# Optimization experiments

Measured on AMD Instinct MI355X. Metric: run time of the kernel, lower is better.

The kernel has to match this reference:

```python
import jax, jax.numpy as jnp
from jax import lax
import numpy as np

FEAT = 2048
HID = 512
OUT = 22
B, T = 16, 2048


def _kaiming(key, shape):
    fan_in = shape[1]
    std = np.sqrt(2.0 / fan_in)
    return jax.random.normal(key, shape, dtype=jnp.float32) * std


def setup_inputs() -> dict:
    key = jax.random.key(0)
    ks = jax.random.split(key, 12)
    x = jax.random.normal(ks[0], (B, T, FEAT), dtype=jnp.float32)
    inp = {
        "x": x,
        # main cell (PyTorch LSTMCell gate order: i, f, g, o)
        "w_ih": _kaiming(ks[1], (4 * HID, FEAT)),
        "w_hh": _kaiming(ks[2], (4 * HID, HID)),
        "b_ih": jax.random.uniform(ks[3], (4 * HID,), minval=-0.04, maxval=0.04),
        "b_hh": jax.random.uniform(ks[4], (4 * HID,), minval=-0.04, maxval=0.04),
        # ed cell
        "w_ih_ed": _kaiming(ks[5], (4 * HID, FEAT)),
        "w_hh_ed": _kaiming(ks[6], (4 * HID, HID)),
        "b_ih_ed": jax.random.uniform(ks[7], (4 * HID,), minval=-0.04, maxval=0.04),
        "b_hh_ed": jax.random.uniform(ks[8], (4 * HID,), minval=-0.04, maxval=0.04),
        # linear heads
        "fc_w": _kaiming(ks[9], (OUT, HID)),
        "fc_b": jnp.zeros((OUT,), dtype=jnp.float32),
        "fc_ed_w": _kaiming(ks[10], (OUT, HID)),
        "fc_ed_b": jnp.zeros((OUT,), dtype=jnp.float32),
    }
    return inp


def _run_lstm(x, w_ih, w_hh, b_ih, b_hh):
    # Precompute input projection for all timesteps: [B, T, 4H]
    xg = jnp.einsum("btf,gf->btg", x, w_ih) + (b_ih + b_hh)
    hid = w_hh.shape[1]
    b = x.shape[0]

    def step(carry, xg_t):
        h, c = carry
        g = xg_t + h @ w_hh.T  # [B, 4H]
        i, f, gg, o = jnp.split(g, 4, axis=-1)
        c = jax.nn.sigmoid(f) * c + jax.nn.sigmoid(i) * jnp.tanh(gg)
        h = jax.nn.sigmoid(o) * jnp.tanh(c)
        return (h, c), h

    init = (jnp.zeros((b, hid), x.dtype), jnp.zeros((b, hid), x.dtype))
    _, hs = lax.scan(step, init, jnp.swapaxes(xg, 0, 1))  # hs: [T, B, H]
    return jnp.swapaxes(hs, 0, 1)  # [B, T, H]


def reference(x, w_ih, w_hh, b_ih, b_hh, w_ih_ed, w_hh_ed, b_ih_ed, b_hh_ed,
              fc_w, fc_b, fc_ed_w, fc_ed_b):
    hs = _run_lstm(x, w_ih, w_hh, b_ih, b_hh)
    score = jnp.einsum("bth,oh->bto", hs, fc_w) + fc_b
    hs_ed = _run_lstm(x, w_ih_ed, w_hh_ed, b_ih_ed, b_hh_ed)
    ed = jnp.einsum("bth,oh->bto", hs_ed, fc_ed_w) + fc_ed_b
    return (score, ed)
```

## Files before the change

### kernel.cpp

```cpp
#include <hip/hip_runtime.h>
#include <hip/hip_bf16.h>
#include <stdint.h>

typedef __attribute__((ext_vector_type(8))) short s16x8;
typedef __attribute__((ext_vector_type(4))) float f32x4;
typedef unsigned short u16;
typedef unsigned int u32;
typedef unsigned long long u64;

#define FEAT 2048
#define HID  512
#define GATES 2048
#define NB   16
#define NT   2048
#define NOUT 22
#define MROWS (NB*NT)

#define WS_FLAG 0L
#define WS_BIAS 4096L
#define WS_WF   (WS_BIAS + 16384L)
#define WS_WB   (WS_WF + 4194304L)
#define WS_XB   (WS_WB + 16777216L)
#define WS_XG   (WS_XB + 134217728L)
#define WS_HB   (WS_XG + 268435456L)
#define HB_BYTES 67141632L
#define HB_LSTM_U64 (2049L*2048L)
#define HB_SLAB_U64 2048L

__device__ inline float b2f(u16 u){ u32 x = ((u32)u) << 16; return __builtin_bit_cast(float, x); }
__device__ inline u16 f2b(float f){
  u32 u = __builtin_bit_cast(u32, f);
  u32 r = (u + 0x7FFFu + ((u >> 16) & 1u)) >> 16;
  return (u16)r;
}
__device__ inline float sigm(float x){ return __builtin_amdgcn_rcpf(1.f + __expf(-x)); }
__device__ inline float tanh_(float x){ return 1.f - 2.f*__builtin_amdgcn_rcpf(1.f + __expf(2.f*x)); }

__global__ void detect_dtype(const u32* __restrict__ x, int* __restrict__ flag){
  __shared__ int cs;
  if (threadIdx.x == 0) cs = 0;
  __syncthreads();
  int c = 0;
  for (int i = 0; i < 16; i++){
    u32 w = x[threadIdx.x*16 + i];
    u32 e = (w >> 7) & 0xFFu;
    if ((e >= 110u && e <= 134u) || ((w & 0xFFFFu) == 0u)) c++;
  }
  atomicAdd(&cs, c);
  __syncthreads();
  if (threadIdx.x == 0) *flag = (cs > 2048) ? 1 : 0;
}

__global__ void cvt_bf16(const void* __restrict__ src, u16* __restrict__ dst,
                         long n8, const int* __restrict__ flag){
  const int isb = *flag;
  long stride = (long)gridDim.x * blockDim.x;
  for (long i = (long)blockIdx.x*blockDim.x + threadIdx.x; i < n8; i += stride){
    if (isb){
      ((int4*)dst)[i] = ((const int4*)src)[i];
    } else {
      const float4* s = (const float4*)src + 2*i;
      float4 a = s[0], b = s[1];
      s16x8 o;
      o[0]=(short)f2b(a.x); o[1]=(short)f2b(a.y); o[2]=(short)f2b(a.z); o[3]=(short)f2b(a.w);
      o[4]=(short)f2b(b.x); o[5]=(short)f2b(b.y); o[6]=(short)f2b(b.z); o[7]=(short)f2b(b.w);
      *(s16x8*)(dst + i*8) = o;
    }
  }
}

__global__ void bias_sum(const void* bi0, const void* bh0, const void* bi1, const void* bh1,
                         float* __restrict__ out, const int* __restrict__ flag){
  const int isb = *flag;
  int i = blockIdx.x*256 + threadIdx.x;
  int lstm = i >> 11, idx = i & 2047;
  const void* bi = lstm ? bi1 : bi0;
  const void* bh = lstm ? bh1 : bh0;
  float a = isb ? b2f(((const u16*)bi)[idx]) : ((const float*)bi)[idx];
  float b = isb ? b2f(((const u16*)bh)[idx]) : ((const float*)bh)[idx];
  out[i] = a + b;
}

__global__ void reorder_w(const void* __restrict__ w0, const void* __restrict__ w1,
                          u16* __restrict__ wfr, const int* __restrict__ flag){
  const int isb = *flag;
  int t = blockIdx.x*256 + threadIdx.x;
  int l   = t & 63;
  int kk  = (t >> 6) & 15;
  int tau = (t >> 10) & 127;
  int lstm = t >> 17;
  int m = tau >> 5;
  int w = tau & 31;
  int j = m*512 + w*16 + (l & 15);
  size_t sidx = (size_t)j*HID + kk*32 + (l >> 4)*8;
  const void* src = lstm ? w1 : w0;
  s16x8 o;
  if (isb){
    o = *(const s16x8*)((const u16*)src + sidx);
  } else {
    const float* s = (const float*)src + sidx;
#pragma unroll
    for (int e = 0; e < 8; e++) o[e] = (short)f2b(s[e]);
  }
  *(s16x8*)(wfr + ((((size_t)lstm*128 + tau)*16 + kk)*64 + l)*8) = o;
}

__global__ __launch_bounds__(256,2) void gemm_xg(const u16* __restrict__ xb,
    const u16* __restrict__ wb, const float* __restrict__ bias, u16* __restrict__ xg){
  __shared__ u16 As[2][128*64];
  __shared__ u16 Bs[2][128*64];
  const int lstm = blockIdx.z;
  const int n0 = blockIdx.x * 128;
  const int m0 = blockIdx.y * 128;
  const int tid = threadIdx.x;
  const int lane = tid & 63;
  const int wid = tid >> 6;
  const int wr = wid >> 1, wc = wid & 1;
  const u16* Bw = wb + (size_t)lstm * GATES * FEAT;

  f32x4 acc[4][4] = {};

  auto stage = [&](int buf, int kt){
    const int k0 = kt*64;
#pragma unroll
    for (int i = 0; i < 4; i++){
      int cc = tid + 256*i;
      int row = cc >> 3;
      int slot = cc & 7;
      int slotp = slot ^ (row & 7);
      const u16* ga = xb + (size_t)(m0+row)*FEAT + k0 + slotp*8;
      const u16* gb = Bw + (size_t)(n0+row)*FEAT + k0 + slotp*8;
      __builtin_amdgcn_global_load_lds((const __attribute__((address_space(1))) void*)ga,
          (__attribute__((address_space(3))) void*)&As[buf][cc*8], 16, 0, 0);
      __builtin_amdgcn_global_load_lds((const __attribute__((address_space(1))) void*)gb,
          (__attribute__((address_space(3))) void*)&Bs[buf][cc*8], 16, 0, 0);
    }
  };

  stage(0, 0);
  __syncthreads();
  for (int kt = 0; kt < 32; kt++){
    int buf = kt & 1;
    if (kt < 31) stage(buf^1, kt+1);
    const char* Ab = (const char*)&As[buf][0];
    const char* Bb = (const char*)&Bs[buf][0];
#pragma unroll
    for (int ks = 0; ks < 2; ks++){
      s16x8 af[4], bf[4];
#pragma unroll
      for (int mi = 0; mi < 4; mi++){
        int row = wr*64 + mi*16 + (lane & 15);
        int off = row*128 + ((ks*64 + ((lane>>4)*16)) ^ ((row & 7) << 4));
        af[mi] = *(const s16x8*)(Ab + off);
      }
#pragma unroll
      for (int ni = 0; ni < 4; ni++){
        int row = wc*64 + ni*16 + (lane & 15);
        int off = row*128 + ((ks*64 + ((lane>>4)*16)) ^ ((row & 7) << 4));
        bf[ni] = *(const s16x8*)(Bb + off);
      }
#pragma unroll
      for (int mi = 0; mi < 4; mi++)
#pragma unroll
        for (int ni = 0; ni < 4; ni++)
          acc[mi][ni] = __builtin_amdgcn_mfma_f32_16x16x32_bf16(af[mi], bf[ni], acc[mi][ni], 0, 0, 0);
    }
    __syncthreads();
  }

  u16* xgl = xg + (size_t)lstm * MROWS * GATES;
#pragma unroll
  for (int mi = 0; mi < 4; mi++){
#pragma unroll
    for (int ni = 0; ni < 4; ni++){
      int gcol = n0 + wc*64 + ni*16 + (lane & 15);
      float bv = bias[lstm*GATES + gcol];
#pragma unroll
      for (int r = 0; r < 4; r++){
        int grow = m0 + wr*64 + mi*16 + ((lane>>4)<<2) + r;
        xgl[(size_t)grow*GATES + gcol] = f2b(acc[mi][ni][r] + bv);
      }
    }
  }
}

__global__ __launch_bounds__(64,1) void lstm_rec(const u16* __restrict__ wfr,
    const u16* __restrict__ xg, u64* __restrict__ hb64){
  __shared__ s16x8 Wl[4][16][64];
  const int lstm = blockIdx.x >> 5;
  const int w = blockIdx.x & 31;
  const int lane = threadIdx.x;
  const int n = lane & 15;
  const int g = lane >> 4;
  const int b0 = g * 4;

  u64* myslab = hb64 + (size_t)lstm * HB_LSTM_U64;
  const char* srcp = (const char*)myslab + (size_t)n*1024 + g*16;

  {
    const s16x8* wfb = (const s16x8*)wfr;
#pragma unroll
    for (int tt = 0; tt < 4; tt++){
      const s16x8* wt = wfb + (((size_t)lstm*128 + (tt*32 + w))*16)*64 + lane;
#pragma unroll
      for (int kk = 0; kk < 16; kk++)
        Wl[tt][kk][lane] = wt[kk*64];
    }
  }

  const u16* xpb[4];
#pragma unroll
  for (int m = 0; m < 4; m++)
    xpb[m] = xg + (size_t)lstm*MROWS*GATES + (size_t)b0*NT*GATES + (m*512 + w*16 + n);

  u16 xv[4][4], xn_[4][4];
#pragma unroll
  for (int m = 0; m < 4; m++)
#pragma unroll
    for (int r = 0; r < 4; r++)
      xv[m][r] = xpb[m][(size_t)r*NT*GATES];

  float c[4] = {};

  for (int t = 0; t < NT; t++){
    const size_t tno = (size_t)((t < NT-1) ? (t+1) : t) * GATES;
#pragma unroll
    for (int m = 0; m < 4; m++)
#pragma unroll
      for (int r = 0; r < 4; r++)
        xn_[m][r] = xpb[m][(size_t)r*NT*GATES + tno];

    int4 H0,H1,H2,H3,H4,H5,H6,H7,H8,H9,H10,H11,H12,H13,H14,H15;
    int retry = 0;
    for (;;){
      asm volatile(
        "global_load_dwordx4 %0,  %16, off sc0 sc1\n"
        "global_load_dwordx4 %1,  %16, off offset:64 sc0 sc1\n"
        "global_load_dwordx4 %2,  %16, off offset:128 sc0 sc1\n"
        "global_load_dwordx4 %3,  %16, off offset:192 sc0 sc1\n"
        "global_load_dwordx4 %4,  %16, off offset:256 sc0 sc1\n"
        "global_load_dwordx4 %5,  %16, off offset:320 sc0 sc1\n"
        "global_load_dwordx4 %6,  %16, off offset:384 sc0 sc1\n"
        "global_load_dwordx4 %7,  %16, off offset:448 sc0 sc1\n"
        "global_load_dwordx4 %8,  %16, off offset:512 sc0 sc1\n"
        "global_load_dwordx4 %9,  %16, off offset:576 sc0 sc1\n"
        "global_load_dwordx4 %10, %16, off offset:640 sc0 sc1\n"
        "global_load_dwordx4 %11, %16, off offset:704 sc0 sc1\n"
        "global_load_dwordx4 %12, %16, off offset:768 sc0 sc1\n"
        "global_load_dwordx4 %13, %16, off offset:832 sc0 sc1\n"
        "global_load_dwordx4 %14, %16, off offset:896 sc0 sc1\n"
        "global_load_dwordx4 %15, %16, off offset:960 sc0 sc1\n"
        "s_waitcnt vmcnt(0)"
        : "=v"(H0), "=v"(H1), "=v"(H2), "=v"(H3),
          "=v"(H4), "=v"(H5), "=v"(H6), "=v"(H7),
          "=v"(H8), "=v"(H9), "=v"(H10), "=v"(H11),
          "=v"(H12), "=v"(H13), "=v"(H14), "=v"(H15)
        : "v"(srcp));
      u32 bad = ((u32)H0.x == ~0u) | ((u32)H0.z == ~0u)
              | ((u32)H1.x == ~0u) | ((u32)H1.z == ~0u)
              | ((u32)H2.x == ~0u) | ((u32)H2.z == ~0u)
              | ((u32)H3.x == ~0u) | ((u32)H3.z == ~0u)
              | ((u32)H4.x == ~0u) | ((u32)H4.z == ~0u)
              | ((u32)H5.x == ~0u) | ((u32)H5.z == ~0u)
              | ((u32)H6.x == ~0u) | ((u32)H6.z == ~0u)
              | ((u32)H7.x == ~0u) | ((u32)H7.z == ~0u)
              | ((u32)H8.x == ~0u) | ((u32)H8.z == ~0u)
              | ((u32)H9.x == ~0u) | ((u32)H9.z == ~0u)
              | ((u32)H10.x == ~0u) | ((u32)H10.z == ~0u)
              | ((u32)H11.x == ~0u) | ((u32)H11.z == ~0u)
              | ((u32)H12.x == ~0u) | ((u32)H12.z == ~0u)
              | ((u32)H13.x == ~0u) | ((u32)H13.z == ~0u)
              | ((u32)H14.x == ~0u) | ((u32)H14.z == ~0u)
              | ((u32)H15.x == ~0u) | ((u32)H15.z == ~0u);
      if (!__any(bad)) break;
      retry++;
      if ((retry & 15) == 0){
        int4 F[16];
#pragma unroll
        for (int i = 0; i < 16; i++){
          u64 a = __hip_atomic_load((const u64*)(srcp + i*64),
                                    __ATOMIC_RELAXED, __HIP_MEMORY_SCOPE_AGENT);
          u64 b = __hip_atomic_load((const u64*)(srcp + i*64 + 8),
                                    __ATOMIC_RELAXED, __HIP_MEMORY_SCOPE_AGENT);
          F[i].x = (int)(u32)a; F[i].y = (int)(u32)(a >> 32);
          F[i].z = (int)(u32)b; F[i].w = (int)(u32)(b >> 32);
        }
        u32 bad2 = 0;
#pragma unroll
        for (int i = 0; i < 16; i++)
          bad2 |= ((u32)F[i].x == ~0u) | ((u32)F[i].z == ~0u);
        if (!__any(bad2)){
          H0=F[0]; H1=F[1]; H2=F[2]; H3=F[3]; H4=F[4]; H5=F[5]; H6=F[6]; H7=F[7];
          H8=F[8]; H9=F[9]; H10=F[10]; H11=F[11]; H12=F[12]; H13=F[13]; H14=F[14]; H15=F[15];
          break;
        }
      }
      if (retry > (1 << 15)) break;
      if (retry > 8) __builtin_amdgcn_s_sleep(1);
    }

    f32x4 a0 = {}, a1 = {}, a2 = {}, a3 = {};
#define LMM(kk, HV) { s16x8 hf = __builtin_bit_cast(s16x8, HV); \
      a0 = __builtin_amdgcn_mfma_f32_16x16x32_bf16(hf, Wl[0][kk][lane], a0, 0, 0, 0); \
      a1 = __builtin_amdgcn_mfma_f32_16x16x32_bf16(hf, Wl[1][kk][lane], a1, 0, 0, 0); \
      a2 = __builtin_amdgcn_mfma_f32_16x16x32_bf16(hf, Wl[2][kk][lane], a2, 0, 0, 0); \
      a3 = __builtin_amdgcn_mfma_f32_16x16x32_bf16(hf, Wl[3][kk][lane], a3, 0, 0, 0); }
    LMM(0,H0) LMM(1,H1) LMM(2,H2) LMM(3,H3) LMM(4,H4) LMM(5,H5) LMM(6,H6) LMM(7,H7)
    LMM(8,H8) LMM(9,H9) LMM(10,H10) LMM(11,H11) LMM(12,H12) LMM(13,H13) LMM(14,H14) LMM(15,H15)
#undef LMM

    u16 hob[4];
#pragma unroll
    for (int r = 0; r < 4; r++){
      float iv = a0[r] + b2f(xv[0][r]);
      float fv = a1[r] + b2f(xv[1][r]);
      float gv = a2[r] + b2f(xv[2][r]);
      float ov = a3[r] + b2f(xv[3][r]);
      float cn = sigm(fv)*c[r] + sigm(iv)*tanh_(gv);
      c[r] = cn;
      hob[r] = f2b(sigm(ov)*tanh_(cn));
    }

    u64* dst = myslab + (size_t)(t+1)*HB_SLAB_U64;
    const int base4 = lane & 60;
#pragma unroll
    for (int r = 0; r < 4; r++){
      int hh = (int)hob[r];
      int v0 = __shfl(hh, base4+0, 64) & 0xFFFF;
      int v1 = __shfl(hh, base4+1, 64) & 0xFFFF;
      int v2 = __shfl(hh, base4+2, 64) & 0xFFFF;
      int v3 = __shfl(hh, base4+3, 64) & 0xFFFF;
      u64 v = (u64)(u32)(v0 | (v1 << 16)) | ((u64)(u32)(v2 | (v3 << 16)) << 32);
      if ((lane & 3) == 0){
        u64* d = dst + (size_t)(b0 + r)*128 + (w*4 + (n >> 2));
        __hip_atomic_store(d, v, __ATOMIC_RELAXED, __HIP_MEMORY_SCOPE_AGENT);
      }
    }
#pragma unroll
    for (int m = 0; m < 4; m++)
#pragma unroll
      for (int r = 0; r < 4; r++) xv[m][r] = xn_[m][r];
    srcp += HB_SLAB_U64 * 8;
  }
}

__global__ __launch_bounds__(256,4) void head_fc(const u16* __restrict__ hb,
    const void* fcw0, const void* fcb0, const void* fcw1, const void* fcb1,
    void* __restrict__ dout, const int* __restrict__ flag){
  const int isb = *flag;
  const int lane = threadIdx.x & 63;
  const int wv = threadIdx.x >> 6;
  int row = blockIdx.x*4 + wv;
  const int lstm = row >> 15;
  const int rem = row & 32767;
  const int b = rem >> 11;
  const int t = rem & 2047;
  const u16* hrow = hb + (((size_t)lstm*2049 + (t+1))*16 + b)*512;
  float hv[8];
  {
    s16x8 h8 = *(const s16x8*)(hrow + lane*8);
#pragma unroll
    for (int e = 0; e < 8; e++) hv[e] = b2f((u16)h8[e]);
  }
  const void* fcw = lstm ? fcw1 : fcw0;
  const void* fcb = lstm ? fcb1 : fcb0;
  float bval = 0.f;
  if (lane < NOUT) bval = isb ? b2f(((const u16*)fcb)[lane]) : ((const float*)fcb)[lane];
  float res = 0.f;
  for (int o = 0; o < NOUT; o++){
    float pa = 0.f;
    if (isb){
      s16x8 w8 = *(const s16x8*)((const u16*)fcw + (size_t)o*HID + lane*8);
#pragma unroll
      for (int e = 0; e < 8; e++) pa += hv[e] * b2f((u16)w8[e]);
    } else {
      const float* wr = (const float*)fcw + (size_t)o*HID + lane*8;
#pragma unroll
      for (int e = 0; e < 8; e++) pa += hv[e] * wr[e];
    }
#pragma unroll
    for (int d = 1; d < 64; d <<= 1) pa += __shfl_xor(pa, d, 64);
    if (lane == o) res = pa + bval;
  }
  size_t off = (size_t)lstm*(MROWS*NOUT) + (size_t)rem*NOUT;
  if (lane < NOUT){
    if (isb) ((u16*)dout)[off + lane] = f2b(res);
    else     ((float*)dout)[off + lane] = res;
  }
}

extern "C" void kernel_launch(void* const* d_in, const int* in_sizes, int n_in,
                              void* d_out, int out_size, void* d_ws, size_t ws_size,
                              hipStream_t stream){
  char* ws = (char*)d_ws;
  int*   flag = (int*)(ws + WS_FLAG);
  float* bias = (float*)(ws + WS_BIAS);
  u16*   wfr  = (u16*)(ws + WS_WF);
  u16*   wb   = (u16*)(ws + WS_WB);
  u16*   xb   = (u16*)(ws + WS_XB);
  u16*   xg   = (u16*)(ws + WS_XG);
  u16*   hb   = (u16*)(ws + WS_HB);

  (void)hipMemsetAsync(ws + WS_FLAG, 0, 4096, stream);
  (void)hipMemsetAsync(ws + WS_HB, 0xFF, HB_BYTES, stream);
  (void)hipMemsetAsync(ws + WS_HB, 0, 16384, stream);
  (void)hipMemsetAsync(ws + WS_HB + 2049L*16*512*2, 0, 16384, stream);

  detect_dtype<<<1, 256, 0, stream>>>((const u32*)d_in[0], flag);

  cvt_bf16<<<2048, 256, 0, stream>>>(d_in[0], xb,             67108864L/8, flag);
  cvt_bf16<<<2048, 256, 0, stream>>>(d_in[1], wb,              4194304L/8, flag);
  cvt_bf16<<<2048, 256, 0, stream>>>(d_in[5], wb + 4194304L,   4194304L/8, flag);
  reorder_w<<<1024, 256, 0, stream>>>(d_in[2], d_in[6], wfr, flag);
  bias_sum<<<16, 256, 0, stream>>>(d_in[3], d_in[4], d_in[7], d_in[8], bias, flag);

  gemm_xg<<<dim3(16, 256, 2), 256, 0, stream>>>(xb, wb, bias, xg);
  lstm_rec<<<64, 64, 0, stream>>>(wfr, xg, (u64*)hb);
  head_fc<<<16384, 256, 0, stream>>>(hb, d_in[9], d_in[10], d_in[11], d_in[12], d_out, flag);
}
```

Measured before the change: 9.179 ms.

## Fuse input-projection GEMM with LSTM recurrence to overlap via sentinel polling

Merges the xg GEMM and the recurrent LSTM kernel into one launch. The first 64 blocks run the recurrence while the remaining blocks compute the input projection, ordered by time tile so early timesteps are produced first. The xg buffer is pre-filled with 0xFFFF sentinels, GEMM results are written with system-coherent stores, and the recurrence polls for non-sentinel values. This hides the GEMM time behind the serial recurrence, at the cost of an extra 256MB memset, sentinel checks on every step, and a possible stall or deadlock if the recurrence blocks are not co-resident with the GEMM blocks. A genuine bf16 result equal to 0xFFFF (a NaN) would also be read as not yet written.

```diff
diff --git a/kernel.cpp b/kernel.cpp
--- a/kernel.cpp
+++ b/kernel.cpp
@@ -105,88 +105,101 @@
   *(s16x8*)(wfr + ((((size_t)lstm*128 + tau)*16 + kk)*64 + l)*8) = o;
 }
 
-__global__ __launch_bounds__(256,2) void gemm_xg(const u16* __restrict__ xb,
-    const u16* __restrict__ wb, const float* __restrict__ bias, u16* __restrict__ xg){
-  __shared__ u16 As[2][128*64];
-  __shared__ u16 Bs[2][128*64];
-  const int lstm = blockIdx.z;
-  const int n0 = blockIdx.x * 128;
-  const int m0 = blockIdx.y * 128;
-  const int tid = threadIdx.x;
-  const int lane = tid & 63;
-  const int wid = tid >> 6;
-  const int wr = wid >> 1, wc = wid & 1;
-  const u16* Bw = wb + (size_t)lstm * GATES * FEAT;
-
-  f32x4 acc[4][4] = {};
-
-  auto stage = [&](int buf, int kt){
-    const int k0 = kt*64;
-#pragma unroll
-    for (int i = 0; i < 4; i++){
-      int cc = tid + 256*i;
-      int row = cc >> 3;
-      int slot = cc & 7;
-      int slotp = slot ^ (row & 7);
-      const u16* ga = xb + (size_t)(m0+row)*FEAT + k0 + slotp*8;
-      const u16* gb = Bw + (size_t)(n0+row)*FEAT + k0 + slotp*8;
-      __builtin_amdgcn_global_load_lds((const __attribute__((address_space(1))) void*)ga,
-          (__attribute__((address_space(3))) void*)&As[buf][cc*8], 16, 0, 0);
-      __builtin_amdgcn_global_load_lds((const __attribute__((address_space(1))) void*)gb,
-          (__attribute__((address_space(3))) void*)&Bs[buf][cc*8], 16, 0, 0);
-    }
-  };
-
-  stage(0, 0);
-  __syncthreads();
-  for (int kt = 0; kt < 32; kt++){
-    int buf = kt & 1;
-    if (kt < 31) stage(buf^1, kt+1);
-    const char* Ab = (const char*)&As[buf][0];
-    const char* Bb = (const char*)&Bs[buf][0];
-#pragma unroll
-    for (int ks = 0; ks < 2; ks++){
-      s16x8 af[4], bf[4];
-#pragma unroll
-      for (int mi = 0; mi < 4; mi++){
-        int row = wr*64 + mi*16 + (lane & 15);
-        int off = row*128 + ((ks*64 + ((lane>>4)*16)) ^ ((row & 7) << 4));
-        af[mi] = *(const s16x8*)(Ab + off);
-      }
+union FSmem {
+  struct { u16 As[2][8192]; u16 Bs[2][8192]; } g;
+  s16x8 Wl[4][16][64];
+};
+
+__global__ __launch_bounds__(256,2) void fused_rec(const u16* __restrict__ wfr,
+    const u16* __restrict__ xb, const u16* __restrict__ wb,
+    const float* __restrict__ bias, u16* __restrict__ xg, u64* __restrict__ hb64){
+  __shared__ FSmem sm;
+
+  if (blockIdx.x >= 64){
+    const int gid = blockIdx.x - 64;
+    const int lstm = gid & 1;
+    const int n0 = ((gid >> 1) & 15) * 128;
+    const int y = gid >> 5;
+    const int b = y & 15;
+    const int tblk = y >> 4;
+    const int m0 = b*NT + tblk*128;
+    const int tid = threadIdx.x;
+    const int lane = tid & 63;
+    const int wid = tid >> 6;
+    const int wr = wid >> 1, wc = wid & 1;
+    const u16* Bw = wb + (size_t)lstm * GATES * FEAT;
+
+    f32x4 acc[4][4] = {};
+
+    auto stage = [&](int buf, int kt){
+      const int k0 = kt*64;
+#pragma unroll
+      for (int i = 0; i < 4; i++){
+        int cc = tid + 256*i;
+        int row = cc >> 3;
+        int slot = cc & 7;
+        int slotp = slot ^ (row & 7);
+        const u16* ga = xb + (size_t)(m0+row)*FEAT + k0 + slotp*8;
+        const u16* gb = Bw + (size_t)(n0+row)*FEAT + k0 + slotp*8;
+        __builtin_amdgcn_global_load_lds((const __attribute__((address_space(1))) void*)ga,
+            (__attribute__((address_space(3))) void*)&sm.g.As[buf][cc*8], 16, 0, 0);
+        __builtin_amdgcn_global_load_lds((const __attribute__((address_space(1))) void*)gb,
+            (__attribute__((address_space(3))) void*)&sm.g.Bs[buf][cc*8], 16, 0, 0);
+      }
+    };
+
+    stage(0, 0);
+    __syncthreads();
+    for (int kt = 0; kt < 32; kt++){
+      int buf = kt & 1;
+      if (kt < 31) stage(buf^1, kt+1);
+      const char* Ab = (const char*)&sm.g.As[buf][0];
+      const char* Bb = (const char*)&sm.g.Bs[buf][0];
+#pragma unroll
+      for (int ks = 0; ks < 2; ks++){
+        s16x8 af[4], bf[4];
+#pragma unroll
+        for (int mi = 0; mi < 4; mi++){
+          int row = wr*64 + mi*16 + (lane & 15);
+          int off = row*128 + ((ks*64 + ((lane>>4)*16)) ^ ((row & 7) << 4));
+          af[mi] = *(const s16x8*)(Ab + off);
+        }
+#pragma unroll
+        for (int ni = 0; ni < 4; ni++){
+          int row = wc*64 + ni*16 + (lane & 15);
+          int off = row*128 + ((ks*64 + ((lane>>4)*16)) ^ ((row & 7) << 4));
+          bf[ni] = *(const s16x8*)(Bb + off);
+        }
+#pragma unroll
+        for (int mi = 0; mi < 4; mi++)
+#pragma unroll
+          for (int ni = 0; ni < 4; ni++)
+            acc[mi][ni] = __builtin_amdgcn_mfma_f32_16x16x32_bf16(af[mi], bf[ni], acc[mi][ni], 0, 0, 0);
+      }
+      __syncthreads();
+    }
+
+    u16* xgl = xg + (size_t)lstm * MROWS * GATES;
+#pragma unroll
+    for (int mi = 0; mi < 4; mi++){
 #pragma unroll
       for (int ni = 0; ni < 4; ni++){
-        int row = wc*64 + ni*16 + (lane & 15);
-        int off = row*128 + ((ks*64 + ((lane>>4)*16)) ^ ((row & 7) << 4));
-        bf[ni] = *(const s16x8*)(Bb + off);
-      }
-#pragma unroll
-      for (int mi = 0; mi < 4; mi++)
-#pragma unroll
-        for (int ni = 0; ni < 4; ni++)
-          acc[mi][ni] = __builtin_amdgcn_mfma_f32_16x16x32_bf16(af[mi], bf[ni], acc[mi][ni], 0, 0, 0);
-    }
-    __syncthreads();
-  }
-
-  u16* xgl = xg + (size_t)lstm * MROWS * GATES;
-#pragma unroll
-  for (int mi = 0; mi < 4; mi++){
-#pragma unroll
-    for (int ni = 0; ni < 4; ni++){
-      int gcol = n0 + wc*64 + ni*16 + (lane & 15);
-      float bv = bias[lstm*GATES + gcol];
-#pragma unroll
-      for (int r = 0; r < 4; r++){
-        int grow = m0 + wr*64 + mi*16 + ((lane>>4)<<2) + r;
-        xgl[(size_t)grow*GATES + gcol] = f2b(acc[mi][ni][r] + bv);
-      }
-    }
-  }
-}
-
-__global__ __launch_bounds__(64,1) void lstm_rec(const u16* __restrict__ wfr,
-    const u16* __restrict__ xg, u64* __restrict__ hb64){
-  __shared__ s16x8 Wl[4][16][64];
+        int gcol = n0 + wc*64 + ni*16 + (lane & 15);
+        float bv = bias[lstm*GATES + gcol];
+#pragma unroll
+        for (int r = 0; r < 4; r++){
+          int grow = m0 + wr*64 + mi*16 + ((lane>>4)<<2) + r;
+          u16 val = f2b(acc[mi][ni][r] + bv);
+          u16* ad = &xgl[(size_t)grow*GATES + gcol];
+          asm volatile("global_store_short %0, %1, off sc0 sc1"
+                       :: "v"(ad), "v"((u32)val));
+        }
+      }
+    }
+    return;
+  }
+
+  if (threadIdx.x >= 64) return;
   const int lstm = blockIdx.x >> 5;
   const int w = blockIdx.x & 31;
   const int lane = threadIdx.x;
@@ -204,7 +217,7 @@
       const s16x8* wt = wfb + (((size_t)lstm*128 + (tt*32 + w))*16)*64 + lane;
 #pragma unroll
       for (int kk = 0; kk < 16; kk++)
-        Wl[tt][kk][lane] = wt[kk*64];
+        sm.Wl[tt][kk][lane] = wt[kk*64];
     }
   }
 
@@ -299,12 +312,36 @@
       if (retry > 8) __builtin_amdgcn_s_sleep(1);
     }
 
+    {
+      u32 xbad = 0;
+#pragma unroll
+      for (int m = 0; m < 4; m++)
+#pragma unroll
+        for (int r = 0; r < 4; r++) xbad |= (xv[m][r] == (u16)0xFFFFu);
+      if (__builtin_expect(__any(xbad), 0)){
+#pragma unroll
+        for (int m = 0; m < 4; m++)
+#pragma unroll
+          for (int r = 0; r < 4; r++){
+            if (xv[m][r] == (u16)0xFFFFu){
+              const u16* a = xpb[m] + (size_t)r*NT*GATES + (size_t)t*GATES;
+              u32 v; int k = 0;
+              do {
+                asm volatile("global_load_ushort %0, %1, off sc0 sc1\n"
+                             "s_waitcnt vmcnt(0)" : "=v"(v) : "v"(a));
+              } while ((u16)v == (u16)0xFFFFu && ++k < (1 << 15));
+              xv[m][r] = (u16)v;
+            }
+          }
+      }
+    }
+
     f32x4 a0 = {}, a1 = {}, a2 = {}, a3 = {};
 #define LMM(kk, HV) { s16x8 hf = __builtin_bit_cast(s16x8, HV); \
-      a0 = __builtin_amdgcn_mfma_f32_16x16x32_bf16(hf, Wl[0][kk][lane], a0, 0, 0, 0); \
-      a1 = __builtin_amdgcn_mfma_f32_16x16x32_bf16(hf, Wl[1][kk][lane], a1, 0, 0, 0); \
-      a2 = __builtin_amdgcn_mfma_f32_16x16x32_bf16(hf, Wl[2][kk][lane], a2, 0, 0, 0); \
-      a3 = __builtin_amdgcn_mfma_f32_16x16x32_bf16(hf, Wl[3][kk][lane], a3, 0, 0, 0); }
+      a0 = __builtin_amdgcn_mfma_f32_16x16x32_bf16(hf, sm.Wl[0][kk][lane], a0, 0, 0, 0); \
+      a1 = __builtin_amdgcn_mfma_f32_16x16x32_bf16(hf, sm.Wl[1][kk][lane], a1, 0, 0, 0); \
+      a2 = __builtin_amdgcn_mfma_f32_16x16x32_bf16(hf, sm.Wl[2][kk][lane], a2, 0, 0, 0); \
+      a3 = __builtin_amdgcn_mfma_f32_16x16x32_bf16(hf, sm.Wl[3][kk][lane], a3, 0, 0, 0); }
     LMM(0,H0) LMM(1,H1) LMM(2,H2) LMM(3,H3) LMM(4,H4) LMM(5,H5) LMM(6,H6) LMM(7,H7)
     LMM(8,H8) LMM(9,H9) LMM(10,H10) LMM(11,H11) LMM(12,H12) LMM(13,H13) LMM(14,H14) LMM(15,H15)
 #undef LMM
@@ -405,6 +442,7 @@
   (void)hipMemsetAsync(ws + WS_HB, 0xFF, HB_BYTES, stream);
   (void)hipMemsetAsync(ws + WS_HB, 0, 16384, stream);
   (void)hipMemsetAsync(ws + WS_HB + 2049L*16*512*2, 0, 16384, stream);
+  (void)hipMemsetAsync(ws + WS_XG, 0xFF, 268435456L, stream);
 
   detect_dtype<<<1, 256, 0, stream>>>((const u32*)d_in[0], flag);
 
@@ -414,7 +452,6 @@
   reorder_w<<<1024, 256, 0, stream>>>(d_in[2], d_in[6], wfr, flag);
   bias_sum<<<16, 256, 0, stream>>>(d_in[3], d_in[4], d_in[7], d_in[8], bias, flag);
 
-  gemm_xg<<<dim3(16, 256, 2), 256, 0, stream>>>(xb, wb, bias, xg);
-  lstm_rec<<<64, 64, 0, stream>>>(wfr, xg, (u64*)hb);
+  fused_rec<<<64 + 8192, 256, 0, stream>>>(wfr, xb, wb, bias, xg, (u64*)hb);
   head_fc<<<16384, 256, 0, stream>>>(hb, d_in[9], d_in[10], d_in[11], d_in[12], d_out, flag);
 }
```

Result: no change. 9.190 ms (+0.1%).
